# Optimization experiments

Hardware: AMD Instinct MI355X
Metric: run time of the kernel (lower is better)

Reference implementation:

```python
import jax, jax.numpy as jnp
import numpy as np
import math

D_MODEL = 768
N_HEAD = 12
D_FF = 3072
LN_EPS = 1e-5


def gelu_new(x):
    return 0.5 * x * (1.0 + jnp.tanh(jnp.sqrt(2.0 / jnp.pi) * (x + 0.044715 * x ** 3)))


def layer_norm(x, g, b):
    mu = jnp.mean(x, axis=-1, keepdims=True)
    var = jnp.mean(jnp.square(x - mu), axis=-1, keepdims=True)
    return (x - mu) * jax.lax.rsqrt(var + LN_EPS) * g + b


def setup_inputs() -> dict:
    key = jax.random.key(0)
    ks = jax.random.split(key, 8)
    B, S = 4, 2048
    x = jax.random.normal(ks[0], (B, S, D_MODEL), dtype=jnp.float32)
    # causal look-ahead mask: 1 = attend, 0 = masked
    look_ahead_mask = jnp.tril(jnp.ones((S, S), dtype=jnp.float32))[None, None]
    std = 0.02
    Wqkv = jax.random.normal(ks[1], (D_MODEL, 3 * D_MODEL), dtype=jnp.float32) * std
    bqkv = jnp.zeros((3 * D_MODEL,), dtype=jnp.float32)
    Wo = jax.random.normal(ks[2], (D_MODEL, D_MODEL), dtype=jnp.float32) * std
    bo = jnp.zeros((D_MODEL,), dtype=jnp.float32)
    Wfc = jax.random.normal(ks[3], (D_MODEL, D_FF), dtype=jnp.float32) * std
    bfc = jnp.zeros((D_FF,), dtype=jnp.float32)
    Wpr = jax.random.normal(ks[4], (D_FF, D_MODEL), dtype=jnp.float32) * std
    bpr = jnp.zeros((D_MODEL,), dtype=jnp.float32)
    g1 = jnp.ones((D_MODEL,), dtype=jnp.float32)
    b1 = jnp.zeros((D_MODEL,), dtype=jnp.float32)
    g2 = jnp.ones((D_MODEL,), dtype=jnp.float32)
    b2 = jnp.zeros((D_MODEL,), dtype=jnp.float32)
    return dict(x=x, look_ahead_mask=look_ahead_mask, Wqkv=Wqkv, bqkv=bqkv,
                Wo=Wo, bo=bo, Wfc=Wfc, bfc=bfc, Wpr=Wpr, bpr=bpr,
                g1=g1, b1=b1, g2=g2, b2=b2)


def reference(x, look_ahead_mask, Wqkv, bqkv, Wo, bo, Wfc, bfc, Wpr, bpr, g1, b1, g2, b2):
    B, S, D = x.shape
    dk = D // N_HEAD
    # --- attention sublayer (dropout = identity, eval mode) ---
    nx = layer_norm(x, g1, b1)
    qkv = nx @ Wqkv + bqkv                       # [B,S,3D]
    q, k, v = jnp.split(qkv, 3, axis=-1)
    def heads(t):
        return t.reshape(B, S, N_HEAD, dk).transpose(0, 2, 1, 3)  # [B,H,S,dk]
    q, k, v = heads(q), heads(k), heads(v)
    scores = jnp.einsum('bhqd,bhkd->bhqk', q, k) / jnp.sqrt(jnp.float32(dk))
    scores = scores + (1.0 - look_ahead_mask) * -10000.0
    attn_scores = jax.nn.softmax(scores, axis=-1)  # [B,H,S,S]
    out = jnp.einsum('bhqk,bhkd->bhqd', attn_scores, v)
    out = out.transpose(0, 2, 1, 3).reshape(B, S, D)
    a = out @ Wo + bo
    x = x + a
    # --- MLP sublayer ---
    h = layer_norm(x, g2, b2)
    m = gelu_new(h @ Wfc + bfc) @ Wpr + bpr
    x = x + m
    return (x, attn_scores)
```

## Files before the change

### kernel.cpp

```cpp
#include <hip/hip_runtime.h>
#include <stdint.h>

#define D_MODEL 768
#define NHEAD   12
#define DKH     64
#define SEQ     2048
#define BATCH   4
#define DFF     3072
#define NROWS   (BATCH*SEQ)

typedef __bf16 bf16x8 __attribute__((ext_vector_type(8)));
typedef float  f32x4  __attribute__((ext_vector_type(4)));

__device__ __forceinline__ unsigned short f2bf(float f) {
  union { float f; unsigned int u; } v; v.f = f;
  unsigned int r = v.u + 0x7fffu + ((v.u >> 16) & 1u);
  return (unsigned short)(r >> 16);
}

__device__ __forceinline__ void gl_lds16(const void* g, void* l) {
  __builtin_amdgcn_global_load_lds(
      (__attribute__((address_space(1))) void*)(uintptr_t)g,
      (__attribute__((address_space(3))) void*)(uintptr_t)l, 16, 0, 0);
}

__global__ __launch_bounds__(256) void k_prep(
    const float* __restrict__ Wqkv, const float* __restrict__ Wo,
    const float* __restrict__ Wfc, const float* __restrict__ Wpr,
    unsigned short* __restrict__ WqkvT, unsigned short* __restrict__ WoT,
    unsigned short* __restrict__ WfcT, unsigned short* __restrict__ WprT,
    const float* __restrict__ x, const float* __restrict__ g1,
    const float* __restrict__ b1, unsigned short* __restrict__ nx) {
  int id = blockIdx.x;
  if (id < NROWS) {
    int row = id, t = threadIdx.x;
    const float* xr = x + (size_t)row * D_MODEL;
    float v0 = xr[t], v1 = xr[t + 256], v2 = xr[t + 512];
    float s = v0 + v1 + v2;
    float s2 = v0 * v0 + v1 * v1 + v2 * v2;
#pragma unroll
    for (int off = 32; off >= 1; off >>= 1) {
      s  += __shfl_xor(s, off, 64);
      s2 += __shfl_xor(s2, off, 64);
    }
    __shared__ float rs_[4], rs2_[4];
    int w = t >> 6;
    if ((t & 63) == 0) { rs_[w] = s; rs2_[w] = s2; }
    __syncthreads();
    s  = rs_[0] + rs_[1] + rs_[2] + rs_[3];
    s2 = rs2_[0] + rs2_[1] + rs2_[2] + rs2_[3];
    float mu  = s * (1.0f / D_MODEL);
    float var = s2 * (1.0f / D_MODEL) - mu * mu;
    float rstd = rsqrtf(var + 1e-5f);
    unsigned short* yr = nx + (size_t)row * D_MODEL;
    yr[t]       = f2bf((v0 - mu) * rstd * g1[t]       + b1[t]);
    yr[t + 256] = f2bf((v1 - mu) * rstd * g1[t + 256] + b1[t + 256]);
    yr[t + 512] = f2bf((v2 - mu) * rstd * g1[t + 512] + b1[t + 512]);
  } else {
    int wid = id - NROWS;
    const float* W; unsigned short* Wt; int K, N, tid;
    if (wid < 1728)      { W = Wqkv; Wt = WqkvT; K = 768;  N = 2304; tid = wid; }
    else if (wid < 2304) { W = Wo;   Wt = WoT;   K = 768;  N = 768;  tid = wid - 1728; }
    else if (wid < 4608) { W = Wfc;  Wt = WfcT;  K = 768;  N = 3072; tid = wid - 2304; }
    else                 { W = Wpr;  Wt = WprT;  K = 3072; N = 768;  tid = wid - 4608; }
    int ntn = N / 32;
    int n0 = (tid % ntn) * 32, k0 = (tid / ntn) * 32;

    __shared__ float tile[32][33];
    int c = threadIdx.x & 31, r = threadIdx.x >> 5;
#pragma unroll
    for (int i = 0; i < 4; ++i)
      tile[r + i * 8][c] = W[(size_t)(k0 + r + i * 8) * N + n0 + c];
    __syncthreads();
#pragma unroll
    for (int i = 0; i < 4; ++i)
      Wt[(size_t)(n0 + r + i * 8) * K + k0 + c] = f2bf(tile[c][r + i * 8]);
  }
}

__global__ __launch_bounds__(256) void k_ln(const float* __restrict__ x,
                                            const float* __restrict__ g,
                                            const float* __restrict__ bb,
                                            unsigned short* __restrict__ y) {
  int row = blockIdx.x, t = threadIdx.x;
  const float* xr = x + (size_t)row * D_MODEL;
  float v0 = xr[t], v1 = xr[t + 256], v2 = xr[t + 512];
  float s = v0 + v1 + v2;
  float s2 = v0 * v0 + v1 * v1 + v2 * v2;
#pragma unroll
  for (int off = 32; off >= 1; off >>= 1) {
    s  += __shfl_xor(s, off, 64);
    s2 += __shfl_xor(s2, off, 64);
  }
  __shared__ float rs_[4], rs2_[4];
  int w = t >> 6;
  if ((t & 63) == 0) { rs_[w] = s; rs2_[w] = s2; }
  __syncthreads();
  s  = rs_[0] + rs_[1] + rs_[2] + rs_[3];
  s2 = rs2_[0] + rs2_[1] + rs2_[2] + rs2_[3];
  float mu  = s * (1.0f / D_MODEL);
  float var = s2 * (1.0f / D_MODEL) - mu * mu;
  float rstd = rsqrtf(var + 1e-5f);
  unsigned short* yr = y + (size_t)row * D_MODEL;
  yr[t]       = f2bf((v0 - mu) * rstd * g[t]       + bb[t]);
  yr[t + 256] = f2bf((v1 - mu) * rstd * g[t + 256] + bb[t + 256]);
  yr[t + 512] = f2bf((v2 - mu) * rstd * g[t + 512] + bb[t + 512]);
}

#define EPI_QKV 0
#define EPI_WO  1
#define EPI_FC  2
#define EPI_PR  3

template <int EPI>
__global__ __launch_bounds__(256) void k_gemm(
    const unsigned short* __restrict__ A,
    const unsigned short* __restrict__ Bt,
    const float* __restrict__ bias,
    const float* __restrict__ res,
    float* __restrict__ outf,
    unsigned short* __restrict__ outb,
    unsigned short* __restrict__ qo,
    unsigned short* __restrict__ ko,
    unsigned short* __restrict__ vto,
    int K, int N) {
  __shared__ __align__(16) unsigned char smem[36864];
  unsigned short* As = (unsigned short*)smem;
  unsigned short* Bs = (unsigned short*)(smem + 16384);
  int t = threadIdx.x;
  int l = t & 63, w = t >> 6;
  int wm = w >> 1, wn = w & 1;

  int gx = gridDim.x;
  int nwg = gx * gridDim.y;
  int orig = blockIdx.y * gx + blockIdx.x;
  int wg = (orig & 7) * (nwg >> 3) + (orig >> 3);
  int bx = wg % gx, by = wg / gx;
  int m0 = by * 128, n0 = bx * 128;
  int lr = l & 15, lg = l >> 4;

  const f32x4 fz = {0.0f, 0.0f, 0.0f, 0.0f};
  f32x4 acc[4][4];
#pragma unroll
  for (int i = 0; i < 4; ++i)
#pragma unroll
    for (int j = 0; j < 4; ++j) acc[i][j] = fz;

  int arow = t >> 3;
  int aslot = t & 7;
  const unsigned short* Ag = A + (size_t)(m0 + arow) * K + aslot * 8;
  const unsigned short* Bg = Bt + (size_t)(n0 + arow) * K + aslot * 8;
  int ntile = K >> 6;

  for (int kt = 0; kt < ntile; ++kt) {
    const unsigned short* Agk = Ag + kt * 64;
    const unsigned short* Bgk = Bg + kt * 64;
#pragma unroll
    for (int i = 0; i < 4; ++i)
      gl_lds16(Agk + (size_t)i * 32 * K, As + (i * 256 + t) * 8);
#pragma unroll
    for (int i = 0; i < 4; ++i)
      gl_lds16(Bgk + (size_t)i * 32 * K, Bs + (i * 256 + t) * 8);
    __syncthreads();
#pragma unroll
    for (int ks = 0; ks < 2; ++ks) {
      bf16x8 af[4], bf_[4];
#pragma unroll
      for (int i = 0; i < 4; ++i)
        af[i] = *(const bf16x8*)(As + (wm * 64 + i * 16 + lr) * 64 + ks * 32 + lg * 8);
#pragma unroll
      for (int i = 0; i < 4; ++i)
        bf_[i] = *(const bf16x8*)(Bs + (wn * 64 + i * 16 + lr) * 64 + ks * 32 + lg * 8);
#pragma unroll
      for (int i = 0; i < 4; ++i)
#pragma unroll
        for (int j = 0; j < 4; ++j)
          acc[i][j] = __builtin_amdgcn_mfma_f32_16x16x32_bf16(af[i], bf_[j], acc[i][j], 0, 0, 0);
    }
    __syncthreads();
  }

  int mb = m0 + wm * 64;
  int nb = n0 + wn * 64;

  if constexpr (EPI == EPI_WO || EPI == EPI_PR) {
#pragma unroll
    for (int i = 0; i < 4; ++i)
#pragma unroll
      for (int r = 0; r < 4; ++r) {
        int m = mb + i * 16 + 4 * lg + r;
#pragma unroll
        for (int j = 0; j < 4; ++j) {
          int n = nb + j * 16 + lr;
          outf[(size_t)m * D_MODEL + n] = acc[i][j][r] + bias[n] + res[(size_t)m * D_MODEL + n];
        }
      }
  } else if constexpr (EPI == EPI_FC) {
#pragma unroll
    for (int i = 0; i < 4; ++i)
#pragma unroll
      for (int r = 0; r < 4; ++r) {
        int m = mb + i * 16 + 4 * lg + r;
#pragma unroll
        for (int j = 0; j < 4; ++j) {
          int n = nb + j * 16 + lr;
          float u = acc[i][j][r] + bias[n];
          float c = 0.7978845608028654f * (u + 0.044715f * u * u * u);
          float a2 = fabsf(c);
          float e = __expf(-2.0f * a2);
          float th = (1.0f - e) / (1.0f + e);
          th = (c < 0.0f) ? -th : th;
          outb[(size_t)m * DFF + n] = f2bf(0.5f * u * (1.0f + th));
        }
      }
  } else {
    int region = n0 / 768;
    int b = m0 >> 11;
    if (region < 2) {
      unsigned short* dst = (region == 0) ? qo : ko;
#pragma unroll
      for (int i = 0; i < 4; ++i)
#pragma unroll
        for (int r = 0; r < 4; ++r) {
          int m = mb + i * 16 + 4 * lg + r;
          int s = m & (SEQ - 1);
#pragma unroll
          for (int j = 0; j < 4; ++j) {
            int n = nb + j * 16 + lr;
            int nl = n - region * 768;
            int h = nl >> 6, d = nl & 63;
            dst[(((size_t)(b * NHEAD + h) * SEQ + s) << 6) + d] = f2bf(acc[i][j][r] + bias[n]);
          }
        }
    } else {
      int nl = nb - 1536;
      int h = nl >> 6;
      unsigned short* Tw = (unsigned short*)(smem + w * 9216);
#pragma unroll
      for (int j = 0; j < 4; ++j) {
        int dcol = j * 16 + lr;
        int n = nb + j * 16 + lr;
#pragma unroll
        for (int i = 0; i < 4; ++i)
#pragma unroll
          for (int r = 0; r < 4; ++r)
            Tw[dcol * 72 + i * 16 + 4 * lg + r] = f2bf(acc[i][j][r] + bias[n]);
      }
      __syncthreads();
      int srow = l >> 3, sc = (l & 7) * 8;
      int s0 = mb & (SEQ - 1);
#pragma unroll
      for (int i = 0; i < 8; ++i) {
        int d = i * 8 + srow;
        bf16x8 vv = *(const bf16x8*)(Tw + d * 72 + sc);
        *(bf16x8*)(vto + ((size_t)(b * NHEAD + h) * DKH + d) * SEQ + s0 + sc) = vv;
      }
    }
  }
}

template <int WRITEP>
__global__ __launch_bounds__(256) void k_attn(const unsigned short* __restrict__ q,
                                              const unsigned short* __restrict__ kk,
                                              const unsigned short* __restrict__ vt,
                                              float* __restrict__ lsumbuf,
                                              float* __restrict__ attn,
                                              unsigned short* __restrict__ ao) {
  __shared__ __align__(16) unsigned short Ks[2][64 * 64];
  __shared__ __align__(16) unsigned short Vts[2][64 * 64];
  __shared__ __align__(16) unsigned short Pw[4][32 * 72];
  int t = threadIdx.x, l = t & 63, w = t >> 6;
  int lr = l & 15, lg = l >> 4;
  int qt = gridDim.x - 1 - blockIdx.x;
  int bh = blockIdx.y;
  int q0 = qt * 128;
  int qrow0 = q0 + w * 32;
  int kmax = 2 * qt + 1;

  auto stageK = [&](int kt, int buf) {
#pragma unroll
    for (int i = 0; i < 2; ++i) {
      int lin = i * 256 + t;
      gl_lds16(kk + ((size_t)bh * SEQ + kt * 64 + (lin >> 3)) * DKH + (lin & 7) * 8,
               Ks[buf] + lin * 8);
    }
  };
  auto stageV = [&](int kt, int buf) {
#pragma unroll
    for (int i = 0; i < 2; ++i) {
      int lin = i * 256 + t;
      gl_lds16(vt + ((size_t)bh * DKH + (lin >> 3)) * SEQ + kt * 64 + (lin & 7) * 8,
               Vts[buf] + lin * 8);
    }
  };

  bf16x8 aq[2][2];
#pragma unroll
  for (int m = 0; m < 2; ++m) {
    const unsigned short* qbase = q + ((size_t)bh * SEQ + qrow0 + m * 16 + lr) * DKH;
    aq[m][0] = *(const bf16x8*)(qbase + lg * 8);
    aq[m][1] = *(const bf16x8*)(qbase + 32 + lg * 8);
  }

  const f32x4 fz = {0.0f, 0.0f, 0.0f, 0.0f};
  float lsum[2][4] = {{0.f, 0.f, 0.f, 0.f}, {0.f, 0.f, 0.f, 0.f}};
  f32x4 oacc[2][4];
#pragma unroll
  for (int m = 0; m < 2; ++m)
#pragma unroll
    for (int f = 0; f < 4; ++f) oacc[m][f] = fz;

  unsigned short* Pme = Pw[w];
  stageK(0, 0);
  stageV(0, 0);
  __syncthreads();
  int cur = 0;
  for (int kt = 0; kt <= kmax; ++kt) {
    if (kt < kmax) { stageK(kt + 1, cur ^ 1); stageV(kt + 1, cur ^ 1); }
    const unsigned short* Kc = Ks[cur];
    const unsigned short* Vc = Vts[cur];
#pragma unroll
    for (int m = 0; m < 2; ++m) {
      f32x4 sacc[4];
#pragma unroll
      for (int f = 0; f < 4; ++f) sacc[f] = fz;
#pragma unroll
      for (int f = 0; f < 4; ++f) {
        bf16x8 bk0 = *(const bf16x8*)(Kc + (f * 16 + lr) * 64 + lg * 8);
        sacc[f] = __builtin_amdgcn_mfma_f32_16x16x32_bf16(aq[m][0], bk0, sacc[f], 0, 0, 0);
        bf16x8 bk1 = *(const bf16x8*)(Kc + (f * 16 + lr) * 64 + 32 + lg * 8);
        sacc[f] = __builtin_amdgcn_mfma_f32_16x16x32_bf16(aq[m][1], bk1, sacc[f], 0, 0, 0);
      }
#pragma unroll
      for (int r = 0; r < 4; ++r) {
        int qg = qrow0 + m * 16 + 4 * lg + r;
        float rsum = 0.f;
#pragma unroll
        for (int f = 0; f < 4; ++f) {
          int ksg = kt * 64 + f * 16 + lr;
          float p = (ksg <= qg) ? __expf(sacc[f][r] * 0.125f) : 0.0f;
          rsum += p;
          Pme[(m * 16 + 4 * lg + r) * 72 + f * 16 + lr] = f2bf(p);
        }
        rsum += __shfl_xor(rsum, 1, 64);
        rsum += __shfl_xor(rsum, 2, 64);
        rsum += __shfl_xor(rsum, 4, 64);
        rsum += __shfl_xor(rsum, 8, 64);
        lsum[m][r] += rsum;
      }
    }
#pragma unroll
    for (int ds = 0; ds < 2; ++ds)
#pragma unroll
      for (int m = 0; m < 2; ++m) {
        bf16x8 ap = *(const bf16x8*)(Pme + (m * 16 + lr) * 72 + ds * 32 + lg * 8);
#pragma unroll
        for (int f = 0; f < 4; ++f) {
          bf16x8 bv = *(const bf16x8*)(Vc + (f * 16 + lr) * 64 + ds * 32 + lg * 8);
          oacc[m][f] = __builtin_amdgcn_mfma_f32_16x16x32_bf16(ap, bv, oacc[m][f], 0, 0, 0);
        }
      }
    __syncthreads();
    cur ^= 1;
  }

  float invl[2][4];
#pragma unroll
  for (int m = 0; m < 2; ++m)
#pragma unroll
    for (int r = 0; r < 4; ++r) {
      invl[m][r] = 1.0f / lsum[m][r];
      if (WRITEP == 0 && lr == 0)
        lsumbuf[(size_t)bh * SEQ + qrow0 + m * 16 + 4 * lg + r] = lsum[m][r];
    }

  int b = bh / NHEAD, h = bh % NHEAD;
#pragma unroll
  for (int m = 0; m < 2; ++m)
#pragma unroll
    for (int r = 0; r < 4; ++r) {
      int qg = qrow0 + m * 16 + 4 * lg + r;
#pragma unroll
      for (int f = 0; f < 4; ++f)
        ao[(size_t)(b * SEQ + qg) * D_MODEL + h * DKH + f * 16 + lr] =
            f2bf(oacc[m][f][r] * invl[m][r]);
    }

  if (WRITEP) {
    stageK(0, 0);
    __syncthreads();
    cur = 0;
    for (int kt = 0; kt <= kmax; ++kt) {
      if (kt < kmax) stageK(kt + 1, cur ^ 1);
      const unsigned short* Kc = Ks[cur];
#pragma unroll
      for (int m = 0; m < 2; ++m) {
        f32x4 sacc[4];
#pragma unroll
        for (int f = 0; f < 4; ++f) sacc[f] = fz;
#pragma unroll
        for (int f = 0; f < 4; ++f) {
          bf16x8 bk0 = *(const bf16x8*)(Kc + (f * 16 + lr) * 64 + lg * 8);
          sacc[f] = __builtin_amdgcn_mfma_f32_16x16x32_bf16(aq[m][0], bk0, sacc[f], 0, 0, 0);
          bf16x8 bk1 = *(const bf16x8*)(Kc + (f * 16 + lr) * 64 + 32 + lg * 8);
          sacc[f] = __builtin_amdgcn_mfma_f32_16x16x32_bf16(aq[m][1], bk1, sacc[f], 0, 0, 0);
        }
#pragma unroll
        for (int r = 0; r < 4; ++r) {
          int qg = qrow0 + m * 16 + 4 * lg + r;
#pragma unroll
          for (int f = 0; f < 4; ++f) {
            int ksg = kt * 64 + f * 16 + lr;
            float p = (ksg <= qg) ? __expf(sacc[f][r] * 0.125f) * invl[m][r] : 0.0f;
            __builtin_nontemporal_store(p, &attn[((size_t)bh * SEQ + qg) * SEQ + ksg]);
          }
        }
      }
      __syncthreads();
      cur ^= 1;
    }

    int zstart = q0 + 128;
    const f32x4 z4 = {0.f, 0.f, 0.f, 0.f};
#pragma unroll
    for (int m = 0; m < 2; ++m)
#pragma unroll
      for (int r = 0; r < 4; ++r) {
        int qg = qrow0 + m * 16 + 4 * lg + r;
        float* rowp = attn + ((size_t)bh * SEQ + qg) * SEQ;
        for (int c = zstart + lr * 4; c < SEQ; c += 64)
          __builtin_nontemporal_store(z4, (f32x4*)(rowp + c));
      }
  }
}

__global__ __launch_bounds__(256) void k_pwrite(const unsigned short* __restrict__ q,
                                                const unsigned short* __restrict__ kk,
                                                const float* __restrict__ lsumbuf,
                                                float* __restrict__ attn) {
  __shared__ __align__(16) unsigned short Ks[64 * 64];
  int t = threadIdx.x, l = t & 63, w = t >> 6;
  int lr = l & 15, lg = l >> 4;
  int qt = blockIdx.x, bh = blockIdx.y;
  int qrow0 = qt * 64 + w * 16;

  const unsigned short* qbase = q + ((size_t)bh * SEQ + qrow0 + lr) * DKH;
  bf16x8 aq0 = *(const bf16x8*)(qbase + lg * 8);
  bf16x8 aq1 = *(const bf16x8*)(qbase + 32 + lg * 8);

  float invl[4];
#pragma unroll
  for (int r = 0; r < 4; ++r)
    invl[r] = 1.0f / lsumbuf[(size_t)bh * SEQ + qrow0 + 4 * lg + r];

  const f32x4 fz = {0.0f, 0.0f, 0.0f, 0.0f};
  for (int kt = 0; kt <= qt; ++kt) {
#pragma unroll
    for (int i = 0; i < 2; ++i) {
      int lin = i * 256 + t;
      gl_lds16(kk + ((size_t)bh * SEQ + kt * 64 + (lin >> 3)) * DKH + (lin & 7) * 8,
               Ks + lin * 8);
    }
    __syncthreads();
    f32x4 sacc[4];
#pragma unroll
    for (int f = 0; f < 4; ++f) sacc[f] = fz;
#pragma unroll
    for (int f = 0; f < 4; ++f) {
      bf16x8 bk0 = *(const bf16x8*)(Ks + (f * 16 + lr) * 64 + lg * 8);
      sacc[f] = __builtin_amdgcn_mfma_f32_16x16x32_bf16(aq0, bk0, sacc[f], 0, 0, 0);
      bf16x8 bk1 = *(const bf16x8*)(Ks + (f * 16 + lr) * 64 + 32 + lg * 8);
      sacc[f] = __builtin_amdgcn_mfma_f32_16x16x32_bf16(aq1, bk1, sacc[f], 0, 0, 0);
    }
#pragma unroll
    for (int r = 0; r < 4; ++r) {
      int qg = qrow0 + 4 * lg + r;
#pragma unroll
      for (int f = 0; f < 4; ++f) {
        int ksg = kt * 64 + f * 16 + lr;
        float p = (ksg <= qg) ? __expf(sacc[f][r] * 0.125f) * invl[r] : 0.0f;
        attn[((size_t)bh * SEQ + qg) * SEQ + ksg] = p;
      }
    }
    __syncthreads();
  }

  int zstart = (qt + 1) * 64;
#pragma unroll
  for (int r = 0; r < 4; ++r) {
    int qg = qrow0 + 4 * lg + r;
    float* rowp = attn + ((size_t)bh * SEQ + qg) * SEQ;
    for (int c = zstart + lr * 4; c < SEQ; c += 64)
      *(f32x4*)(rowp + c) = fz;
  }
}

extern "C" void kernel_launch(void* const* d_in, const int* in_sizes, int n_in,
                              void* d_out, int out_size, void* d_ws, size_t ws_size,
                              hipStream_t stream) {
  (void)in_sizes; (void)n_in; (void)out_size;
  const float* x    = (const float*)d_in[0];
  const float* Wqkv = (const float*)d_in[2];
  const float* bqkv = (const float*)d_in[3];
  const float* Wo   = (const float*)d_in[4];
  const float* bo   = (const float*)d_in[5];
  const float* Wfc  = (const float*)d_in[6];
  const float* bfc  = (const float*)d_in[7];
  const float* Wpr  = (const float*)d_in[8];
  const float* bpr  = (const float*)d_in[9];
  const float* g1   = (const float*)d_in[10];
  const float* b1   = (const float*)d_in[11];
  const float* g2   = (const float*)d_in[12];
  const float* b2   = (const float*)d_in[13];

  float* outx = (float*)d_out;
  float* attn = outx + (size_t)NROWS * D_MODEL;

  char* ws = (char*)d_ws;
  dim3 blk(256);

  const size_t NEED_FUSED = 77070336;
  if (ws_size >= NEED_FUSED + 65536) {
    unsigned short* qb    = (unsigned short*)(ws + 0);
    unsigned short* kb    = (unsigned short*)(ws + 12582912);
    unsigned short* vtb   = (unsigned short*)(ws + 25165824);
    unsigned short* m1    = (unsigned short*)(ws + 0);
    unsigned short* nx    = (unsigned short*)(ws + 50331648);
    unsigned short* ao    = (unsigned short*)(ws + 50331648);
    unsigned short* hb    = (unsigned short*)(ws + 50331648);
    unsigned short* WqkvT = (unsigned short*)(ws + 62914560);
    unsigned short* WoT   = (unsigned short*)(ws + 66453504);
    unsigned short* WfcT  = (unsigned short*)(ws + 67633152);
    unsigned short* WprT  = (unsigned short*)(ws + 72351744);
    float*          x1    = outx;

    k_prep<<<dim3(NROWS + 6912), blk, 0, stream>>>(
        Wqkv, Wo, Wfc, Wpr, WqkvT, WoT, WfcT, WprT, x, g1, b1, nx);
    k_gemm<EPI_QKV><<<dim3(18, 64), blk, 0, stream>>>(
        nx, WqkvT, bqkv, nullptr, nullptr, nullptr, qb, kb, vtb, 768, 2304);
    k_attn<1><<<dim3(SEQ / 128, BATCH * NHEAD), blk, 0, stream>>>(
        qb, kb, vtb, nullptr, attn, ao);
    k_gemm<EPI_WO><<<dim3(6, 64), blk, 0, stream>>>(
        ao, WoT, bo, x, x1, nullptr, nullptr, nullptr, nullptr, 768, 768);
    k_ln<<<NROWS, blk, 0, stream>>>(x1, g2, b2, hb);
    k_gemm<EPI_FC><<<dim3(24, 64), blk, 0, stream>>>(
        hb, WfcT, bfc, nullptr, nullptr, m1, nullptr, nullptr, nullptr, 768, 3072);
    k_gemm<EPI_PR><<<dim3(6, 64), blk, 0, stream>>>(
        m1, WprT, bpr, x1, outx, nullptr, nullptr, nullptr, nullptr, 3072, 768);
  } else {
    size_t off = 0;
    auto alloc = [&](size_t bytes) {
      char* p = ws + off;
      off += (bytes + 255) & ~(size_t)255;
      return p;
    };
    unsigned short* qb   = (unsigned short*)alloc((size_t)NROWS * D_MODEL * 2);
    unsigned short* kb   = (unsigned short*)alloc((size_t)NROWS * D_MODEL * 2);
    float*          lsum = (float*)alloc((size_t)BATCH * NHEAD * SEQ * 4);

    char* aws = (char*)attn;
    size_t aoff = 0;
    auto aalloc = [&](size_t bytes) {
      char* p = aws + aoff;
      aoff += (bytes + 255) & ~(size_t)255;
      return p;
    };
    unsigned short* WqkvT = (unsigned short*)aalloc((size_t)2304 * 768 * 2);
    unsigned short* WoT   = (unsigned short*)aalloc((size_t)768 * 768 * 2);
    unsigned short* WfcT  = (unsigned short*)aalloc((size_t)3072 * 768 * 2);
    unsigned short* WprT  = (unsigned short*)aalloc((size_t)768 * 3072 * 2);
    unsigned short* nx    = (unsigned short*)aalloc((size_t)NROWS * D_MODEL * 2);
    unsigned short* vtb   = (unsigned short*)aalloc((size_t)NROWS * D_MODEL * 2);
    unsigned short* ao    = (unsigned short*)aalloc((size_t)NROWS * D_MODEL * 2);
    float*          x1    = (float*)aalloc((size_t)NROWS * D_MODEL * 4);
    unsigned short* hb    = (unsigned short*)aalloc((size_t)NROWS * D_MODEL * 2);
    unsigned short* m1    = (unsigned short*)aalloc((size_t)NROWS * DFF * 2);

    k_prep<<<dim3(NROWS + 6912), blk, 0, stream>>>(
        Wqkv, Wo, Wfc, Wpr, WqkvT, WoT, WfcT, WprT, x, g1, b1, nx);
    k_gemm<EPI_QKV><<<dim3(18, 64), blk, 0, stream>>>(
        nx, WqkvT, bqkv, nullptr, nullptr, nullptr, qb, kb, vtb, 768, 2304);
    k_attn<0><<<dim3(SEQ / 128, BATCH * NHEAD), blk, 0, stream>>>(
        qb, kb, vtb, lsum, nullptr, ao);
    k_gemm<EPI_WO><<<dim3(6, 64), blk, 0, stream>>>(
        ao, WoT, bo, x, x1, nullptr, nullptr, nullptr, nullptr, 768, 768);
    k_ln<<<NROWS, blk, 0, stream>>>(x1, g2, b2, hb);
    k_gemm<EPI_FC><<<dim3(24, 64), blk, 0, stream>>>(
        hb, WfcT, bfc, nullptr, nullptr, m1, nullptr, nullptr, nullptr, 768, 3072);
    k_gemm<EPI_PR><<<dim3(6, 64), blk, 0, stream>>>(
        m1, WprT, bpr, x1, outx, nullptr, nullptr, nullptr, nullptr, 3072, 768);

    k_pwrite<<<dim3(SEQ / 64, BATCH * NHEAD), blk, 0, stream>>>(qb, kb, lsum, attn);
  }
}
```

Baseline: 528.8 us.

## Overlap attention-probability writes with MLP GEMMs in shared launches

Adds a combined kernel that runs the attention-probability recompute-and-write blocks alongside the FC and projection GEMM blocks in a single launch, splitting the 1536 pwrite tiles between the two MLP GEMMs. The aim is to hide the bandwidth-bound 805MB attn write behind compute-bound GEMM work, instead of running it serially. A new workspace layout keeps q/k/lsum alive through the MLP. This needs a larger workspace, and it risks the two block types competing for caches and memory bandwidth.

```diff
diff --git a/kernel.cpp b/kernel.cpp
--- a/kernel.cpp
+++ b/kernel.cpp
@@ -259,6 +259,170 @@
   }
 }
 
+template <int EPI>
+__global__ __launch_bounds__(256) void k_gemm_pw(
+    const unsigned short* __restrict__ A,
+    const unsigned short* __restrict__ Bt,
+    const float* __restrict__ bias,
+    const float* __restrict__ res,
+    float* __restrict__ outf,
+    unsigned short* __restrict__ outb,
+    int K, int N,
+    int npw, int gxe, int pwoff,
+    const unsigned short* __restrict__ qp,
+    const unsigned short* __restrict__ kp,
+    const float* __restrict__ lsumbuf,
+    float* __restrict__ attn) {
+  __shared__ __align__(16) unsigned char smem[36864];
+  int t = threadIdx.x;
+  int l = t & 63, w = t >> 6;
+  int lr = l & 15, lg = l >> 4;
+  const f32x4 fz = {0.0f, 0.0f, 0.0f, 0.0f};
+
+  if ((int)blockIdx.x < npw) {
+    unsigned short* Ks = (unsigned short*)smem;
+    int idx = blockIdx.x + pwoff;
+    int qt = 31 - (idx & 31);
+    int bh = idx >> 5;
+    int qrow0 = qt * 64 + w * 16;
+
+    const unsigned short* qbase = qp + ((size_t)bh * SEQ + qrow0 + lr) * DKH;
+    bf16x8 aq0 = *(const bf16x8*)(qbase + lg * 8);
+    bf16x8 aq1 = *(const bf16x8*)(qbase + 32 + lg * 8);
+
+    float invl[4];
+#pragma unroll
+    for (int r = 0; r < 4; ++r)
+      invl[r] = 1.0f / lsumbuf[(size_t)bh * SEQ + qrow0 + 4 * lg + r];
+
+    for (int kt = 0; kt <= qt; ++kt) {
+#pragma unroll
+      for (int i = 0; i < 2; ++i) {
+        int lin = i * 256 + t;
+        gl_lds16(kp + ((size_t)bh * SEQ + kt * 64 + (lin >> 3)) * DKH + (lin & 7) * 8,
+                 Ks + lin * 8);
+      }
+      __syncthreads();
+      f32x4 sacc[4];
+#pragma unroll
+      for (int f = 0; f < 4; ++f) sacc[f] = fz;
+#pragma unroll
+      for (int f = 0; f < 4; ++f) {
+        bf16x8 bk0 = *(const bf16x8*)(Ks + (f * 16 + lr) * 64 + lg * 8);
+        sacc[f] = __builtin_amdgcn_mfma_f32_16x16x32_bf16(aq0, bk0, sacc[f], 0, 0, 0);
+        bf16x8 bk1 = *(const bf16x8*)(Ks + (f * 16 + lr) * 64 + 32 + lg * 8);
+        sacc[f] = __builtin_amdgcn_mfma_f32_16x16x32_bf16(aq1, bk1, sacc[f], 0, 0, 0);
+      }
+#pragma unroll
+      for (int r = 0; r < 4; ++r) {
+        int qg = qrow0 + 4 * lg + r;
+#pragma unroll
+        for (int f = 0; f < 4; ++f) {
+          int ksg = kt * 64 + f * 16 + lr;
+          float p = (ksg <= qg) ? __expf(sacc[f][r] * 0.125f) * invl[r] : 0.0f;
+          __builtin_nontemporal_store(p, &attn[((size_t)bh * SEQ + qg) * SEQ + ksg]);
+        }
+      }
+      __syncthreads();
+    }
+
+    int zstart = (qt + 1) * 64;
+    const f32x4 z4 = {0.f, 0.f, 0.f, 0.f};
+#pragma unroll
+    for (int r = 0; r < 4; ++r) {
+      int qg = qrow0 + 4 * lg + r;
+      float* rowp = attn + ((size_t)bh * SEQ + qg) * SEQ;
+      for (int c = zstart + lr * 4; c < SEQ; c += 64)
+        __builtin_nontemporal_store(z4, (f32x4*)(rowp + c));
+    }
+    return;
+  }
+
+  unsigned short* As = (unsigned short*)smem;
+  unsigned short* Bs = (unsigned short*)(smem + 16384);
+  int wm = w >> 1, wn = w & 1;
+  int orig = blockIdx.x - npw;
+  int ngemm = gridDim.x - npw;
+  int wg = (orig & 7) * (ngemm >> 3) + (orig >> 3);
+  int bx = wg % gxe, by = wg / gxe;
+  int m0 = by * 128, n0 = bx * 128;
+
+  f32x4 acc[4][4];
+#pragma unroll
+  for (int i = 0; i < 4; ++i)
+#pragma unroll
+    for (int j = 0; j < 4; ++j) acc[i][j] = fz;
+
+  int arow = t >> 3;
+  int aslot = t & 7;
+  const unsigned short* Ag = A + (size_t)(m0 + arow) * K + aslot * 8;
+  const unsigned short* Bg = Bt + (size_t)(n0 + arow) * K + aslot * 8;
+  int ntile = K >> 6;
+
+  for (int kt = 0; kt < ntile; ++kt) {
+    const unsigned short* Agk = Ag + kt * 64;
+    const unsigned short* Bgk = Bg + kt * 64;
+#pragma unroll
+    for (int i = 0; i < 4; ++i)
+      gl_lds16(Agk + (size_t)i * 32 * K, As + (i * 256 + t) * 8);
+#pragma unroll
+    for (int i = 0; i < 4; ++i)
+      gl_lds16(Bgk + (size_t)i * 32 * K, Bs + (i * 256 + t) * 8);
+    __syncthreads();
+#pragma unroll
+    for (int ks = 0; ks < 2; ++ks) {
+      bf16x8 af[4], bf_[4];
+#pragma unroll
+      for (int i = 0; i < 4; ++i)
+        af[i] = *(const bf16x8*)(As + (wm * 64 + i * 16 + lr) * 64 + ks * 32 + lg * 8);
+#pragma unroll
+      for (int i = 0; i < 4; ++i)
+        bf_[i] = *(const bf16x8*)(Bs + (wn * 64 + i * 16 + lr) * 64 + ks * 32 + lg * 8);
+#pragma unroll
+      for (int i = 0; i < 4; ++i)
+#pragma unroll
+        for (int j = 0; j < 4; ++j)
+          acc[i][j] = __builtin_amdgcn_mfma_f32_16x16x32_bf16(af[i], bf_[j], acc[i][j], 0, 0, 0);
+    }
+    __syncthreads();
+  }
+
+  int mb = m0 + wm * 64;
+  int nb = n0 + wn * 64;
+
+  if constexpr (EPI == EPI_PR) {
+#pragma unroll
+    for (int i = 0; i < 4; ++i)
+#pragma unroll
+      for (int r = 0; r < 4; ++r) {
+        int m = mb + i * 16 + 4 * lg + r;
+#pragma unroll
+        for (int j = 0; j < 4; ++j) {
+          int n = nb + j * 16 + lr;
+          outf[(size_t)m * D_MODEL + n] = acc[i][j][r] + bias[n] + res[(size_t)m * D_MODEL + n];
+        }
+      }
+  } else {
+#pragma unroll
+    for (int i = 0; i < 4; ++i)
+#pragma unroll
+      for (int r = 0; r < 4; ++r) {
+        int m = mb + i * 16 + 4 * lg + r;
+#pragma unroll
+        for (int j = 0; j < 4; ++j) {
+          int n = nb + j * 16 + lr;
+          float u = acc[i][j][r] + bias[n];
+          float c = 0.7978845608028654f * (u + 0.044715f * u * u * u);
+          float a2 = fabsf(c);
+          float e = __expf(-2.0f * a2);
+          float th = (1.0f - e) / (1.0f + e);
+          th = (c < 0.0f) ? -th : th;
+          outb[(size_t)m * DFF + n] = f2bf(0.5f * u * (1.0f + th));
+        }
+      }
+  }
+}
+
 template <int WRITEP>
 __global__ __launch_bounds__(256) void k_attn(const unsigned short* __restrict__ q,
                                               const unsigned short* __restrict__ kk,
@@ -519,8 +683,40 @@
   char* ws = (char*)d_ws;
   dim3 blk(256);
 
-  const size_t NEED_FUSED = 77070336;
-  if (ws_size >= NEED_FUSED + 65536) {
+  const size_t NEED_A = 102629376;
+  const size_t NEED_B = 77070336;
+
+  if (ws_size >= NEED_A + 65536) {
+    unsigned short* qb    = (unsigned short*)(ws + 0);
+    unsigned short* kb    = (unsigned short*)(ws + 12582912);
+    unsigned short* vtb   = (unsigned short*)(ws + 25165824);
+    unsigned short* m1    = (unsigned short*)(ws + 25165824);
+    unsigned short* nx    = (unsigned short*)(ws + 75497472);
+    unsigned short* ao    = (unsigned short*)(ws + 75497472);
+    unsigned short* hb    = (unsigned short*)(ws + 75497472);
+    unsigned short* WqkvT = (unsigned short*)(ws + 88080384);
+    unsigned short* WoT   = (unsigned short*)(ws + 91619328);
+    unsigned short* WfcT  = (unsigned short*)(ws + 92798976);
+    unsigned short* WprT  = (unsigned short*)(ws + 97517568);
+    float*          lsum  = (float*)(ws + 102236160);
+    float*          x1    = outx;
+
+    k_prep<<<dim3(NROWS + 6912), blk, 0, stream>>>(
+        Wqkv, Wo, Wfc, Wpr, WqkvT, WoT, WfcT, WprT, x, g1, b1, nx);
+    k_gemm<EPI_QKV><<<dim3(18, 64), blk, 0, stream>>>(
+        nx, WqkvT, bqkv, nullptr, nullptr, nullptr, qb, kb, vtb, 768, 2304);
+    k_attn<0><<<dim3(SEQ / 128, BATCH * NHEAD), blk, 0, stream>>>(
+        qb, kb, vtb, lsum, nullptr, ao);
+    k_gemm<EPI_WO><<<dim3(6, 64), blk, 0, stream>>>(
+        ao, WoT, bo, x, x1, nullptr, nullptr, nullptr, nullptr, 768, 768);
+    k_ln<<<NROWS, blk, 0, stream>>>(x1, g2, b2, hb);
+    k_gemm_pw<EPI_FC><<<dim3(768 + 1536), blk, 0, stream>>>(
+        hb, WfcT, bfc, nullptr, nullptr, m1, 768, 3072,
+        768, 24, 0, qb, kb, lsum, attn);
+    k_gemm_pw<EPI_PR><<<dim3(768 + 384), blk, 0, stream>>>(
+        m1, WprT, bpr, x1, outx, nullptr, 3072, 768,
+        768, 6, 768, qb, kb, lsum, attn);
+  } else if (ws_size >= NEED_B + 65536) {
     unsigned short* qb    = (unsigned short*)(ws + 0);
     unsigned short* kb    = (unsigned short*)(ws + 12582912);
     unsigned short* vtb   = (unsigned short*)(ws + 25165824);
@@ -590,6 +786,6 @@
     k_gemm<EPI_PR><<<dim3(6, 64), blk, 0, stream>>>(
         m1, WprT, bpr, x1, outx, nullptr, nullptr, nullptr, nullptr, 3072, 768);
 
-    k_pwrite<<<dim3(SEQ / 64, BATCH * NHEAD), blk, 0, stream>>>(qb, kb, lsum, attn);
-  }
-}
+    k_pwrite<<<dim3(32, BATCH * NHEAD), blk, 0, stream>>>(qb, kb, lsum, attn);
+  }
+}
```

Measured after the change: 574.4 us. 1.09x slower.
